# Performance work log

Hardware: AMD Instinct MI355X
Metric: run time of the kernel (lower is better)

Reference implementation:

```python
import jax, jax.numpy as jnp
import numpy as np

K = 12          # tagset size incl START/STOP
START = 10
STOP = 11
NEG = -10000.0
B, T, V, D, H = 64, 1024, 50000, 256, 512
Hh = H // 2


def setup_inputs() -> dict:
    key = jax.random.key(0)
    ks = jax.random.split(key, 20)
    sentence = jax.random.randint(ks[0], (B, T), 1, V)
    seq_lens = jax.random.randint(ks[1], (B,), T // 2, T + 1)
    emb = jax.random.normal(ks[2], (V, D), dtype=jnp.float32) * 0.1
    emb = emb.at[0].set(0.0)  # padding_idx=0
    s = 1.0 / np.sqrt(Hh)

    def u(k, shape):
        return jax.random.uniform(k, shape, minval=-s, maxval=s, dtype=jnp.float32)

    Wih_f = u(ks[3], (4 * Hh, D)); Whh_f = u(ks[4], (4 * Hh, Hh))
    bih_f = u(ks[5], (4 * Hh,));  bhh_f = u(ks[6], (4 * Hh,))
    Wih_b = u(ks[7], (4 * Hh, D)); Whh_b = u(ks[8], (4 * Hh, Hh))
    bih_b = u(ks[9], (4 * Hh,));  bhh_b = u(ks[10], (4 * Hh,))
    sl = 1.0 / np.sqrt(H)
    Wtag = jax.random.uniform(ks[11], (K, H), minval=-sl, maxval=sl, dtype=jnp.float32)
    btag = jax.random.uniform(ks[12], (K,), minval=-sl, maxval=sl, dtype=jnp.float32)
    transitions = jax.random.normal(ks[13], (K, K), dtype=jnp.float32)
    transitions = transitions.at[START, :].set(NEG).at[:, STOP].set(NEG)
    h0 = jax.random.normal(ks[14], (2, B, Hh), dtype=jnp.float32)
    c0 = jax.random.normal(ks[15], (2, B, Hh), dtype=jnp.float32)
    return dict(sentence=sentence, seq_lens=seq_lens, emb=emb,
                Wih_f=Wih_f, Whh_f=Whh_f, bih_f=bih_f, bhh_f=bhh_f,
                Wih_b=Wih_b, Whh_b=Whh_b, bih_b=bih_b, bhh_b=bhh_b,
                Wtag=Wtag, btag=btag, transitions=transitions, h0=h0, c0=c0)


def _lstm_dir(x, mask, h0, c0, Wih, Whh, bih, bhh, reverse):
    # x: [B,T,D], mask: [B,T] bool. Masked steps keep the carried state
    # (equivalent to PyTorch packed-sequence semantics for positions < seq_len).
    def step(carry, inp):
        h, c = carry
        xt, mt = inp  # [B,D], [B,1]
        z = xt @ Wih.T + h @ Whh.T + bih + bhh  # [B,4Hh], torch gate order i,f,g,o
        i, f, g, o = jnp.split(z, 4, axis=-1)
        c2 = jax.nn.sigmoid(f) * c + jax.nn.sigmoid(i) * jnp.tanh(g)
        h2 = jax.nn.sigmoid(o) * jnp.tanh(c2)
        h = jnp.where(mt, h2, h)
        c = jnp.where(mt, c2, c)
        return (h, c), h
    xs = (x.transpose(1, 0, 2), mask.T[:, :, None])
    _, hs = jax.lax.scan(step, (h0, c0), xs, reverse=reverse)
    return hs.transpose(1, 0, 2)  # [B,T,Hh]


def reference(sentence, seq_lens, emb, Wih_f, Whh_f, bih_f, bhh_f,
              Wih_b, Whh_b, bih_b, bhh_b, Wtag, btag, transitions, h0, c0):
    Bn, Tn = sentence.shape
    mask = jnp.arange(Tn)[None, :] < seq_lens[:, None]  # [B,T]
    x = emb[sentence]  # [B,T,D]
    hf = _lstm_dir(x, mask, h0[0], c0[0], Wih_f, Whh_f, bih_f, bhh_f, False)
    hb = _lstm_dir(x, mask, h0[1], c0[1], Wih_b, Whh_b, bih_b, bhh_b, True)
    feats = jnp.concatenate([hf, hb], -1) @ Wtag.T + btag  # [B,T,K]

    # Vectorized Viterbi over batch and tags (replaces per-tag python loops)
    fv0 = jnp.full((Bn, K), NEG, dtype=feats.dtype).at[:, START].set(0.0)
    ident = jnp.arange(K)[None, :]

    def vstep(fv, inp):
        ft, mt = inp  # [B,K], [B]
        sc = fv[:, None, :] + transitions[None, :, :]  # [B,Knext,Kprev]
        bp = jnp.argmax(sc, -1)                        # [B,K]
        vmax = jnp.max(sc, -1) + ft
        fv2 = jnp.where(mt[:, None], vmax, fv)
        bp = jnp.where(mt[:, None], bp, ident)         # identity passthrough on pad
        return fv2, bp

    fv, bptrs = jax.lax.scan(vstep, fv0, (feats.transpose(1, 0, 2), mask.T))
    term = fv + transitions[STOP][None, :]
    best = jnp.argmax(term, -1)   # [B]
    score = jnp.max(term, -1)     # [B]

    def btrace(tag, bp):
        prev = jnp.take_along_axis(bp, tag[:, None], 1)[:, 0]
        return prev, tag

    _, path = jax.lax.scan(btrace, best, bptrs, reverse=True)  # [T,B]
    path = jnp.where(mask, path.T, 0)  # [B,T], zeros beyond seq_len
    return score, path
```

## Files before the change

kernel.cpp:

```cpp
#include <hip/hip_runtime.h>
#include <math.h>

#define NEG10K -10000.0f

static const size_t OFF_WT_IH = 0;
static const size_t OFF_WT_HH = 524288;
static const size_t OFF_BIAS  = 1048576;
static const size_t OFF_WTAGD = 1050624;
static const size_t OFF_BTAG  = 1058816;
static const size_t OFF_FEATS = 1058832;
static const size_t OFF_HC    = 3155984;
static const size_t OFF_CC    = 3188752;
static const size_t OFF_PUB   = 3221520;
static const size_t OFF_END   = 3352592;

__device__ __forceinline__ float sigf(float x) { return 1.0f / (1.0f + expf(-x)); }

__global__ __launch_bounds__(256) void k_transpose(
    const float* __restrict__ wih_f, const float* __restrict__ wih_b,
    const float* __restrict__ whh_f, const float* __restrict__ whh_b,
    float* __restrict__ ws) {
  __shared__ float tile[32][33];
  int z = blockIdx.z;
  const float* src = (z == 0) ? wih_f : (z == 1) ? wih_b : (z == 2) ? whh_f : whh_b;
  float* dst = ws + ((z < 2) ? (OFF_WT_IH + (size_t)z * 262144)
                             : (OFF_WT_HH + (size_t)(z - 2) * 262144));
  int r0 = blockIdx.y * 32;
  int c0 = blockIdx.x * 32;
  int tid = threadIdx.x;
  int c = tid & 31, rg = tid >> 5;
#pragma unroll
  for (int i = 0; i < 4; ++i) {
    int r = rg * 4 + i;
    tile[r][c] = src[(size_t)(r0 + r) * 256 + c0 + c];
  }
  __syncthreads();
  int r2 = tid & 31, cg = tid >> 5;
#pragma unroll
  for (int i = 0; i < 4; ++i) {
    int ccv = cg * 4 + i;
    dst[(size_t)(c0 + ccv) * 1024 + r0 + r2] = tile[r2][ccv];
  }
}

__global__ __launch_bounds__(256) void k_prep_small(
    const float* __restrict__ bih_f, const float* __restrict__ bhh_f,
    const float* __restrict__ bih_b, const float* __restrict__ bhh_b,
    const float* __restrict__ wtag, const float* __restrict__ btag,
    float* __restrict__ ws) {
  int i = blockIdx.x * 256 + threadIdx.x;
  if (i < 2048) {
    int d = i >> 10, n = i & 1023;
    ws[OFF_BIAS + i] = d ? (bih_b[n] + bhh_b[n]) : (bih_f[n] + bhh_f[n]);
  } else if (i < 2048 + 8192) {
    int r = i - 2048;
    int d = r >> 12, rem = r & 4095;
    int k = rem >> 8, j = rem & 255;
    ws[OFF_WTAGD + r] = (k < 12) ? wtag[(size_t)k * 512 + d * 256 + j] : 0.0f;
  } else if (i < 2048 + 8192 + 16) {
    int kk = i - 10240;
    ws[OFF_BTAG + kk] = (kk < 12) ? btag[kk] : 0.0f;
  } else if (i < 10256 + 131072) {
    ws[OFF_PUB + (i - 10256)] = 0.0f;
  }
}

#define FMA4(A, W, S) { A.x = fmaf(W.x, S, A.x); A.y = fmaf(W.y, S, A.y); \
                        A.z = fmaf(W.z, S, A.z); A.w = fmaf(W.w, S, A.w); }
#define KEEP4(V) asm volatile("" :: "v"(V.x), "v"(V.y), "v"(V.z), "v"(V.w))
__global__ __launch_bounds__(512, 2) void k_lstm_split(
    const float* __restrict__ ws_c, const int* __restrict__ sentence,
    const float* __restrict__ emb, const float* __restrict__ h0p,
    const float* __restrict__ c0p, const int* __restrict__ seq_lens,
    float* __restrict__ ws_mut, int first) {
  __shared__ float zpart[8][4][128];
  __shared__ float zs[4][128];
  __shared__ float h_s[4][256];
  __shared__ float x_s[2][4][256];
  __shared__ int   sent_s[4][1024];
  __shared__ float ldspad[10240];

  int bx = blockIdx.x;
  int w   = (bx >> 3) & 7;
  int gid = (bx & 7) + ((bx >> 6) << 3);
  int d   = gid >> 4;
  int bq4 = (gid & 15) * 4;
  int u0  = w * 32;
  int tid = threadIdx.x;
  if (first == 777) {
    ldspad[tid] = (float)tid; __syncthreads(); zs[0][0] = ldspad[tid ^ 1];
  }

  int cg = tid & 31, kq = tid >> 5;
  int c4 = cg * 4;
  int wv = tid >> 6, ln = tid & 63;

  for (int i = tid; i < 4096; i += 512)
    sent_s[i >> 10][i & 1023] = sentence[(size_t)(bq4 + (i >> 10)) * 1024 + (i & 1023)];
  __syncthreads();

  const float* WhhT = ws_c + OFF_WT_HH + (size_t)d * 262144;
  const float* WihT = ws_c + OFF_WT_IH + (size_t)d * 262144;
  int wcol = (cg >> 3) * 256 + u0 + (cg & 7) * 4;
  float4 wh[16], wi[16];
#pragma unroll
  for (int i = 0; i < 16; ++i) {
    wh[i] = *(const float4*)(WhhT + (size_t)(kq * 16 + i) * 1024 + wcol);
    wi[i] = *(const float4*)(WihT + (size_t)(kq * 16 + i) * 1024 + wcol);
  }

  for (int i = tid; i < 1024; i += 512) {
    int b = i >> 8, u = i & 255;
    h_s[b][u] = h0p[((size_t)d * 64 + bq4 + b) * 256 + u];
  }
  float cc = 0.0f; int mylen = 0;
  int ob = tid >> 5, ou = tid & 31;
  if (tid < 128) {
    cc = c0p[((size_t)d * 64 + bq4 + ob) * 256 + u0 + ou];
    mylen = seq_lens[bq4 + ob];
  }
  int bB = tid >> 7, jB = tid & 127;
  int colB = ((jB >> 5) << 8) + u0 + (jB & 31);
  float biasB = ws_c[OFF_BIAS + (size_t)d * 1024 + colB];
  int xb = tid >> 7, xj = (tid & 127) * 2;
  {
    int tt = d ? 1023 : 0;
    float2 v = *(const float2*)(emb + (size_t)sent_s[xb][tt] * 256 + xj);
    x_s[0][xb][xj] = v.x; x_s[0][xb][xj + 1] = v.y;
  }
  int tb_b = wv >> 1;
  int tb_k = (wv & 1) * 8 + (ln >> 3);
  int tb_j = ln & 7;
  float wtag_r[32];
  {
    const float* wtg = ws_c + OFF_WTAGD + (size_t)d * 4096 + tb_k * 256;
#pragma unroll
    for (int i = 0; i < 32; ++i) wtag_r[i] = wtg[tb_j + 8 * i];
  }
  unsigned long long* pub64 = (unsigned long long*)(ws_mut + OFF_PUB);
  float* featsD = ws_mut + OFF_FEATS + (size_t)d * 1048576;
  int gb = tid >> 8, gu = tid & 255;
  bool bail = false;
  __syncthreads();

  float4 acc_carry[4] = {{0,0,0,0},{0,0,0,0},{0,0,0,0},{0,0,0,0}};
#pragma unroll
  for (int i = 0; i < 4; ++i) {
    int k = kq * 16 + i * 4;
    float4 q0 = wi[i * 4], q1 = wi[i * 4 + 1], q2 = wi[i * 4 + 2], q3 = wi[i * 4 + 3];
#pragma unroll
    for (int b = 0; b < 4; ++b) {
      float4 xv = *(const float4*)&x_s[0][b][k];
      FMA4(acc_carry[b], q0, xv.x); FMA4(acc_carry[b], q1, xv.y);
      FMA4(acc_carry[b], q2, xv.z); FMA4(acc_carry[b], q3, xv.w);
    }
  }

  for (int s = 0; s < 1024; ++s) {
#pragma unroll
    for (int i = 0; i < 16; ++i) { KEEP4(wh[i]); KEEP4(wi[i]); }
    int t = d ? (1023 - s) : s;
    int p = s & 1;
    int nxt = (s & 1) ^ 1;
    unsigned tag = (unsigned)(s + 1);
    float2 xpf;
    {
      int sn = (s + 1 < 1024) ? (s + 1) : s;
      int tn = d ? (1023 - sn) : sn;
      xpf = *(const float2*)(emb + (size_t)sent_s[xb][tn] * 256 + xj);
    }
    float4 acc[4];
#pragma unroll
    for (int b = 0; b < 4; ++b) acc[b] = acc_carry[b];
#pragma unroll
    for (int i = 0; i < 4; ++i) {
      int k = kq * 16 + i * 4;
      float4 w0 = wh[i * 4], w1 = wh[i * 4 + 1], w2 = wh[i * 4 + 2], w3 = wh[i * 4 + 3];
#pragma unroll
      for (int b = 0; b < 4; ++b) {
        float4 hv = *(const float4*)&h_s[b][k];
        FMA4(acc[b], w0, hv.x); FMA4(acc[b], w1, hv.y);
        FMA4(acc[b], w2, hv.z); FMA4(acc[b], w3, hv.w);
      }
    }
#pragma unroll
    for (int b = 0; b < 4; ++b) {
      acc[b].x += __shfl_xor(acc[b].x, 32);
      acc[b].y += __shfl_xor(acc[b].y, 32);
      acc[b].z += __shfl_xor(acc[b].z, 32);
      acc[b].w += __shfl_xor(acc[b].w, 32);
    }
    if ((tid & 32) == 0) {
#pragma unroll
      for (int b = 0; b < 4; ++b) *(float4*)&zpart[wv][b][c4] = acc[b];
    }
    __syncthreads();
    zs[bB][jB] = zpart[0][bB][jB] + zpart[1][bB][jB] + zpart[2][bB][jB] + zpart[3][bB][jB] +
                 zpart[4][bB][jB] + zpart[5][bB][jB] + zpart[6][bB][jB] + zpart[7][bB][jB] + biasB;
    x_s[nxt][xb][xj] = xpf.x; x_s[nxt][xb][xj + 1] = xpf.y;
    __syncthreads();
    if (tid < 128) {
      float zi = zs[ob][ou], zf = zs[ob][32 + ou], zg = zs[ob][64 + ou], zo = zs[ob][96 + ou];
      float cn = sigf(zf) * cc + sigf(zi) * tanhf(zg);
      float hn = sigf(zo) * tanhf(cn);
      bool m = t < mylen;
      cc = m ? cn : cc;
      float hp = m ? hn : h_s[ob][u0 + ou];
      union { float f; unsigned u; } hb; hb.f = hp;
      unsigned long long pk = ((unsigned long long)tag << 32) | (unsigned long long)hb.u;
      __hip_atomic_store(
          pub64 + (size_t)p * 32768 + ((size_t)d * 64 + bq4 + ob) * 256 + (u0 + ou),
          pk, __ATOMIC_RELAXED, __HIP_MEMORY_SCOPE_AGENT);
    }
    if (s > 0) {
      int tp = d ? (1023 - (s - 1)) : (s - 1);
      float pv = 0.0f;
#pragma unroll
      for (int i = 0; i < 32; ++i)
        pv = fmaf(h_s[tb_b][tb_j + 8 * i], wtag_r[i], pv);
      pv += __shfl_xor(pv, 1);
      pv += __shfl_xor(pv, 2);
      pv += __shfl_xor(pv, 4);
      if (w == 0 && tb_j == 0)
        featsD[(size_t)(bq4 + tb_b) * 16384 + (size_t)tp * 16 + tb_k] = pv;
    }
    __syncthreads();
    {
      size_t base = (size_t)p * 32768 + ((size_t)d * 64 + bq4) * 256;
      size_t i0 = base + (size_t)gb * 256 + gu;
      size_t i1 = i0 + 512;
      unsigned long long v0 =
          __hip_atomic_load(pub64 + i0, __ATOMIC_RELAXED, __HIP_MEMORY_SCOPE_AGENT);
      unsigned long long v1 =
          __hip_atomic_load(pub64 + i1, __ATOMIC_RELAXED, __HIP_MEMORY_SCOPE_AGENT);
      if (s + 1 < 1024) {
#pragma unroll
        for (int b = 0; b < 4; ++b) { acc_carry[b].x = 0; acc_carry[b].y = 0;
                                      acc_carry[b].z = 0; acc_carry[b].w = 0; }
#pragma unroll
        for (int i = 0; i < 4; ++i) {
          int k = kq * 16 + i * 4;
          float4 q0 = wi[i * 4], q1 = wi[i * 4 + 1], q2 = wi[i * 4 + 2], q3 = wi[i * 4 + 3];
#pragma unroll
          for (int b = 0; b < 4; ++b) {
            float4 xv = *(const float4*)&x_s[nxt][b][k];
            FMA4(acc_carry[b], q0, xv.x); FMA4(acc_carry[b], q1, xv.y);
            FMA4(acc_carry[b], q2, xv.z); FMA4(acc_carry[b], q3, xv.w);
          }
        }
      }
      unsigned spin = 0;
      while ((((unsigned)(v0 >> 32) != tag) || ((unsigned)(v1 >> 32) != tag)) && !bail) {
        __builtin_amdgcn_s_sleep(1);
        if ((unsigned)(v0 >> 32) != tag)
          v0 = __hip_atomic_load(pub64 + i0, __ATOMIC_RELAXED, __HIP_MEMORY_SCOPE_AGENT);
        if ((unsigned)(v1 >> 32) != tag)
          v1 = __hip_atomic_load(pub64 + i1, __ATOMIC_RELAXED, __HIP_MEMORY_SCOPE_AGENT);
        if (++spin > 2000000u) { bail = true; break; }
      }
      union { unsigned u32; float f; } cv0, cv1;
      cv0.u32 = (unsigned)v0; cv1.u32 = (unsigned)v1;
      h_s[gb][gu]     = cv0.f;
      h_s[gb + 2][gu] = cv1.f;
    }
    __syncthreads();
  }
  {
    float pv = 0.0f;
#pragma unroll
    for (int i = 0; i < 32; ++i)
      pv = fmaf(h_s[tb_b][tb_j + 8 * i], wtag_r[i], pv);
    pv += __shfl_xor(pv, 1);
    pv += __shfl_xor(pv, 2);
    pv += __shfl_xor(pv, 4);
    int tl = d ? 0 : 1023;
    if (w == 0 && tb_j == 0)
      featsD[(size_t)(bq4 + tb_b) * 16384 + (size_t)tl * 16 + tb_k] = pv;
  }
}

__global__ __launch_bounds__(256) void k_lstm_fused(
    const float* __restrict__ ws_c, const int* __restrict__ sentence,
    const float* __restrict__ emb, const float* __restrict__ h0p,
    const float* __restrict__ c0p, const int* __restrict__ seq_lens,
    float* __restrict__ ws_mut) {
  int d = blockIdx.x & 1;
  int pr = blockIdx.x >> 1;
  int b0 = pr * 2, b1 = b0 + 1;
  const float* Wih = ws_c + OFF_WT_IH + (size_t)d * 262144;
  const float* Whh = ws_c + OFF_WT_HH + (size_t)d * 262144;
  __shared__ float h_s[2][256];
  __shared__ float x_s[2][2][256];
  __shared__ float z_s[2][1024];
  __shared__ int   sent_s[2][1024];
  __shared__ float wt_s[16][260];
  __shared__ float pfp_s[2][16][8];
  int tid = threadIdx.x;
  int len0 = seq_lens[b0], len1 = seq_lens[b1];
  for (int i = tid; i < 2048; i += 256)
    sent_s[i >> 10][i & 1023] = sentence[(size_t)(b0 + (i >> 10)) * 1024 + (i & 1023)];
  for (int i = tid; i < 4096; i += 256)
    wt_s[i >> 8][i & 255] = ws_c[OFF_WTAGD + (size_t)d * 4096 + i];
  h_s[0][tid] = h0p[((size_t)d * 64 + b0) * 256 + tid];
  h_s[1][tid] = h0p[((size_t)d * 64 + b1) * 256 + tid];
  float cc0 = c0p[((size_t)d * 64 + b0) * 256 + tid];
  float cc1 = c0p[((size_t)d * 64 + b1) * 256 + tid];
  int c4 = tid * 4;
  float4 bias_v = *(const float4*)(ws_c + OFF_BIAS + (size_t)d * 1024 + c4);
  __syncthreads();
  int t0 = d ? 1023 : 0;
  if (tid < 128) {
    int bb = tid >> 6, l = tid & 63;
    int row = sent_s[bb][t0];
    *(float4*)&x_s[0][bb][l * 4] = *(const float4*)(emb + (size_t)row * 256 + l * 4);
  }
  __syncthreads();
  float* featsD = ws_mut + OFF_FEATS + (size_t)d * 1048576;
  for (int s = 0; s < 1024; ++s) {
    int t = d ? (1023 - s) : s;
    int cur = s & 1, nxt = cur ^ 1;
    float4 pf = {0, 0, 0, 0};
    if (tid < 128) {
      int sn = (s < 1023) ? (s + 1) : 1023;
      int tn = d ? (1023 - sn) : sn;
      int bb = tid >> 6, l = tid & 63;
      pf = *(const float4*)(emb + (size_t)sent_s[bb][tn] * 256 + l * 4);
    }
    float4 a0 = bias_v, a1 = bias_v;
#pragma unroll 4
    for (int k = 0; k < 256; k += 4) {
      float4 xv0 = *(const float4*)&x_s[cur][0][k];
      float4 xv1 = *(const float4*)&x_s[cur][1][k];
      float4 hv0 = *(const float4*)&h_s[0][k];
      float4 hv1 = *(const float4*)&h_s[1][k];
      const float* wi = Wih + (size_t)k * 1024 + c4;
      const float* wh = Whh + (size_t)k * 1024 + c4;
      float4 wi0 = *(const float4*)(wi);
      float4 wi1 = *(const float4*)(wi + 1024);
      float4 wi2 = *(const float4*)(wi + 2048);
      float4 wi3 = *(const float4*)(wi + 3072);
      float4 wh0 = *(const float4*)(wh);
      float4 wh1 = *(const float4*)(wh + 1024);
      float4 wh2 = *(const float4*)(wh + 2048);
      float4 wh3 = *(const float4*)(wh + 3072);
      FMA4(a0, wi0, xv0.x); FMA4(a0, wi1, xv0.y); FMA4(a0, wi2, xv0.z); FMA4(a0, wi3, xv0.w);
      FMA4(a0, wh0, hv0.x); FMA4(a0, wh1, hv0.y); FMA4(a0, wh2, hv0.z); FMA4(a0, wh3, hv0.w);
      FMA4(a1, wi0, xv1.x); FMA4(a1, wi1, xv1.y); FMA4(a1, wi2, xv1.z); FMA4(a1, wi3, xv1.w);
      FMA4(a1, wh0, hv1.x); FMA4(a1, wh1, hv1.y); FMA4(a1, wh2, hv1.z); FMA4(a1, wh3, hv1.w);
    }
    *(float4*)&z_s[0][c4] = a0;
    *(float4*)&z_s[1][c4] = a1;
    __syncthreads();
    {
      float iv = z_s[0][tid], fv = z_s[0][tid + 256];
      float gv = z_s[0][tid + 512], ov = z_s[0][tid + 768];
      float cn = sigf(fv) * cc0 + sigf(iv) * tanhf(gv);
      float hn = sigf(ov) * tanhf(cn);
      bool m = t < len0;
      cc0 = m ? cn : cc0;
      h_s[0][tid] = m ? hn : h_s[0][tid];
    }
    {
      float iv = z_s[1][tid], fv = z_s[1][tid + 256];
      float gv = z_s[1][tid + 512], ov = z_s[1][tid + 768];
      float cn = sigf(fv) * cc1 + sigf(iv) * tanhf(gv);
      float hn = sigf(ov) * tanhf(cn);
      bool m = t < len1;
      cc1 = m ? cn : cc1;
      h_s[1][tid] = m ? hn : h_s[1][tid];
    }
    if (tid < 128) {
      int bb = tid >> 6, l = tid & 63;
      *(float4*)&x_s[nxt][bb][l * 4] = pf;
    }
    __syncthreads();
    {
      int b2 = tid >> 7, r = tid & 127;
      int ks = r >> 3, jg = r & 7;
      const float* hv = &h_s[b2][jg * 32];
      const float* wv = &wt_s[ks][jg * 32];
      float p = 0.0f;
#pragma unroll
      for (int i = 0; i < 32; ++i) p = fmaf(hv[i], wv[i], p);
      pfp_s[b2][ks][jg] = p;
    }
    __syncthreads();
    if (tid < 32) {
      int b = tid >> 4, k = tid & 15;
      float sum = 0.0f;
#pragma unroll
      for (int i = 0; i < 8; ++i) sum += pfp_s[b][k][i];
      featsD[(size_t)(b0 + b) * 16384 + (size_t)t * 16 + k] = sum;
    }
  }
}

__global__ __launch_bounds__(64) void k_viterbi(const float* __restrict__ ws_c,
                                                const float* __restrict__ trans,
                                                const int* __restrict__ seq_lens,
                                                float* __restrict__ out) {
  __shared__ char bp_s[1024][12];
  int b = blockIdx.x, lane = threadIdx.x;
  int len = seq_lens[b];
  float trow[12];
#pragma unroll
  for (int p = 0; p < 12; ++p) trow[p] = (lane < 12) ? trans[lane * 12 + p] : 0.0f;
  float tb = (lane < 16) ? ws_c[OFF_BTAG + lane] : 0.0f;
  float fv = (lane == 10) ? 0.0f : NEG10K;
  const float* ff = ws_c + OFF_FEATS + (size_t)b * 16384;
  const float* fb = ws_c + OFF_FEATS + 1048576 + (size_t)b * 16384;
  for (int t = 0; t < 1024; ++t) {
    float ft = (lane < 16) ? (ff[t * 16 + lane] + fb[t * 16 + lane] + tb) : 0.0f;
    float best = -3.0e38f; int arg = 0;
#pragma unroll
    for (int p = 0; p < 12; ++p) {
      float s = __shfl(fv, p) + trow[p];
      if (s > best) { best = s; arg = p; }
    }
    bool m = t < len;
    if (m) fv = best + ft;
    if (lane < 12) bp_s[t][lane] = (char)(m ? arg : lane);
  }
  float term = (lane < 12) ? fv + trans[132 + lane] : -3.0e38f;
  float bestv = -3.0e38f; int bestp = 0;
#pragma unroll
  for (int p = 0; p < 12; ++p) {
    float v = __shfl(term, p);
    if (v > bestv) { bestv = v; bestp = p; }
  }
  __syncthreads();
  if (lane == 0) {
    out[b] = bestv;
    int tag = bestp;
    float* po = out + 64 + (size_t)b * 1024;
    for (int t = 1023; t >= 0; --t) {
      po[t] = (t < len) ? (float)tag : 0.0f;
      tag = bp_s[t][tag];
    }
  }
}

extern "C" void kernel_launch(void* const* d_in, const int* in_sizes, int n_in,
                              void* d_out, int out_size, void* d_ws, size_t ws_size,
                              hipStream_t stream) {
  (void)in_sizes; (void)n_in; (void)out_size;
  const int*   sentence = (const int*)d_in[0];
  const int*   seq_lens = (const int*)d_in[1];
  const float* emb      = (const float*)d_in[2];
  const float* wih_f    = (const float*)d_in[3];
  const float* whh_f    = (const float*)d_in[4];
  const float* bih_f    = (const float*)d_in[5];
  const float* bhh_f    = (const float*)d_in[6];
  const float* wih_b    = (const float*)d_in[7];
  const float* whh_b    = (const float*)d_in[8];
  const float* bih_b    = (const float*)d_in[9];
  const float* bhh_b    = (const float*)d_in[10];
  const float* wtag     = (const float*)d_in[11];
  const float* btag     = (const float*)d_in[12];
  const float* trans    = (const float*)d_in[13];
  const float* h0p      = (const float*)d_in[14];
  const float* c0p      = (const float*)d_in[15];
  float* ws  = (float*)d_ws;
  float* out = (float*)d_out;
  size_t avail = ws_size / 4;
  if (avail < OFF_FEATS + 2097152) return;

  k_transpose<<<dim3(8, 32, 4), 256, 0, stream>>>(wih_f, wih_b, whh_f, whh_b, ws);
  k_prep_small<<<553, 256, 0, stream>>>(bih_f, bhh_f, bih_b, bhh_b, wtag, btag, ws);
  if (avail >= OFF_END) {
    k_lstm_split<<<256, 512, 0, stream>>>(ws, sentence, emb, h0p, c0p, seq_lens, ws, 1);
  } else {
    k_lstm_fused<<<64, 256, 0, stream>>>(ws, sentence, emb, h0p, c0p, seq_lens, ws);
  }
  k_viterbi<<<64, 64, 0, stream>>>(ws, trans, seq_lens, out);
}
```

Before: 3.628 ms.

## Move input-projection weights from registers to LDS and drop sentence staging

The Wih slice each block uses (256x128 floats, 128KB) now sits in shared memory and is read with float4 LDS loads, instead of living in 64 VGPRs per thread pinned by asm keeps. The sentence tile in shared memory and the dummy LDS padding are removed, and tokens are read straight from global memory each step. This frees register pressure for the Whh path but adds LDS traffic to the per-step input projection and a global token load on the recurrence path. With 128KB of LDS per block, occupancy is likely limited to one block per CU despite launch_bounds(512,2), which could break the co-residency the spin-wait scheme depends on.

```diff
diff --git a/kernel.cpp b/kernel.cpp
--- a/kernel.cpp
+++ b/kernel.cpp
@@ -73,12 +73,11 @@
     const float* __restrict__ emb, const float* __restrict__ h0p,
     const float* __restrict__ c0p, const int* __restrict__ seq_lens,
     float* __restrict__ ws_mut, int first) {
+  __shared__ float wi_s[256][128];
   __shared__ float zpart[8][4][128];
   __shared__ float zs[4][128];
   __shared__ float h_s[4][256];
   __shared__ float x_s[2][4][256];
-  __shared__ int   sent_s[4][1024];
-  __shared__ float ldspad[10240];
 
   int bx = blockIdx.x;
   int w   = (bx >> 3) & 7;
@@ -87,27 +86,23 @@
   int bq4 = (gid & 15) * 4;
   int u0  = w * 32;
   int tid = threadIdx.x;
-  if (first == 777) {
-    ldspad[tid] = (float)tid; __syncthreads(); zs[0][0] = ldspad[tid ^ 1];
-  }
 
   int cg = tid & 31, kq = tid >> 5;
   int c4 = cg * 4;
   int wv = tid >> 6, ln = tid & 63;
 
-  for (int i = tid; i < 4096; i += 512)
-    sent_s[i >> 10][i & 1023] = sentence[(size_t)(bq4 + (i >> 10)) * 1024 + (i & 1023)];
-  __syncthreads();
-
   const float* WhhT = ws_c + OFF_WT_HH + (size_t)d * 262144;
   const float* WihT = ws_c + OFF_WT_IH + (size_t)d * 262144;
+  for (int idx = tid; idx < 32768; idx += 512) {
+    int k = idx >> 7, c = idx & 127;
+    wi_s[k][c] = WihT[(size_t)k * 1024 + (c >> 5) * 256 + u0 + (c & 31)];
+  }
+
   int wcol = (cg >> 3) * 256 + u0 + (cg & 7) * 4;
-  float4 wh[16], wi[16];
-#pragma unroll
-  for (int i = 0; i < 16; ++i) {
+  float4 wh[16];
+#pragma unroll
+  for (int i = 0; i < 16; ++i)
     wh[i] = *(const float4*)(WhhT + (size_t)(kq * 16 + i) * 1024 + wcol);
-    wi[i] = *(const float4*)(WihT + (size_t)(kq * 16 + i) * 1024 + wcol);
-  }
 
   for (int i = tid; i < 1024; i += 512) {
     int b = i >> 8, u = i & 255;
@@ -123,9 +118,10 @@
   int colB = ((jB >> 5) << 8) + u0 + (jB & 31);
   float biasB = ws_c[OFF_BIAS + (size_t)d * 1024 + colB];
   int xb = tid >> 7, xj = (tid & 127) * 2;
+  const int* sent_b = sentence + (size_t)(bq4 + xb) * 1024;
   {
-    int tt = d ? 1023 : 0;
-    float2 v = *(const float2*)(emb + (size_t)sent_s[xb][tt] * 256 + xj);
+    int tok0 = sent_b[d ? 1023 : 0];
+    float2 v = *(const float2*)(emb + (size_t)tok0 * 256 + xj);
     x_s[0][xb][xj] = v.x; x_s[0][xb][xj + 1] = v.y;
   }
   int tb_b = wv >> 1;
@@ -140,6 +136,7 @@
   unsigned long long* pub64 = (unsigned long long*)(ws_mut + OFF_PUB);
   float* featsD = ws_mut + OFF_FEATS + (size_t)d * 1048576;
   int gb = tid >> 8, gu = tid & 255;
+  int ccol = (cg >> 3) * 32 + (cg & 7) * 4;
   bool bail = false;
   __syncthreads();
 
@@ -147,7 +144,10 @@
 #pragma unroll
   for (int i = 0; i < 4; ++i) {
     int k = kq * 16 + i * 4;
-    float4 q0 = wi[i * 4], q1 = wi[i * 4 + 1], q2 = wi[i * 4 + 2], q3 = wi[i * 4 + 3];
+    float4 q0 = *(const float4*)&wi_s[k][ccol];
+    float4 q1 = *(const float4*)&wi_s[k + 1][ccol];
+    float4 q2 = *(const float4*)&wi_s[k + 2][ccol];
+    float4 q3 = *(const float4*)&wi_s[k + 3][ccol];
 #pragma unroll
     for (int b = 0; b < 4; ++b) {
       float4 xv = *(const float4*)&x_s[0][b][k];
@@ -158,7 +158,7 @@
 
   for (int s = 0; s < 1024; ++s) {
 #pragma unroll
-    for (int i = 0; i < 16; ++i) { KEEP4(wh[i]); KEEP4(wi[i]); }
+    for (int i = 0; i < 16; ++i) KEEP4(wh[i]);
     int t = d ? (1023 - s) : s;
     int p = s & 1;
     int nxt = (s & 1) ^ 1;
@@ -167,7 +167,8 @@
     {
       int sn = (s + 1 < 1024) ? (s + 1) : s;
       int tn = d ? (1023 - sn) : sn;
-      xpf = *(const float2*)(emb + (size_t)sent_s[xb][tn] * 256 + xj);
+      int tok = sent_b[tn];
+      xpf = *(const float2*)(emb + (size_t)tok * 256 + xj);
     }
     float4 acc[4];
 #pragma unroll
@@ -240,7 +241,10 @@
 #pragma unroll
         for (int i = 0; i < 4; ++i) {
           int k = kq * 16 + i * 4;
-          float4 q0 = wi[i * 4], q1 = wi[i * 4 + 1], q2 = wi[i * 4 + 2], q3 = wi[i * 4 + 3];
+          float4 q0 = *(const float4*)&wi_s[k][ccol];
+          float4 q1 = *(const float4*)&wi_s[k + 1][ccol];
+          float4 q2 = *(const float4*)&wi_s[k + 2][ccol];
+          float4 q3 = *(const float4*)&wi_s[k + 3][ccol];
 #pragma unroll
           for (int b = 0; b < 4; ++b) {
             float4 xv = *(const float4*)&x_s[nxt][b][k];
@@ -277,6 +281,7 @@
     if (w == 0 && tb_j == 0)
       featsD[(size_t)(bq4 + tb_b) * 16384 + (size_t)tl * 16 + tb_k] = pv;
   }
+  (void)first;
 }
 
 __global__ __launch_bounds__(256) void k_lstm_fused(
```

Result: slower. 3.759 ms (+3.6%).
